# Kernel optimization log

Hardware: AMD Instinct MI355X
Metric: run time of the kernel (lower is better)

Reference implementation:

```python
import jax, jax.numpy as jnp
import numpy as np

N_NODES = 50000
N_EDGES = 800000
NDIM_IN = 64
EDIM = 64
HID = 152  # size_embedding
NDIM_OUT = 64


def _linear(x, W, b):
    # torch nn.Linear: y = x @ W.T + b
    return jnp.matmul(x, W.T) + b


def _sage_layer(nf, ef, Wm, bm, Wa, ba, src, dst):
    # message: gather src node feats, concat edge feats, linear -> [E,1,F]
    m = _linear(jnp.concatenate([nf[src], ef], axis=2), Wm, bm)
    # mean scatter-reduce to dst nodes (zero for nodes with no in-edges)
    s = jax.ops.segment_sum(m, dst, num_segments=N_NODES)
    deg = jax.ops.segment_sum(jnp.ones((m.shape[0],), m.dtype), dst, num_segments=N_NODES)
    h_neigh = s / jnp.maximum(deg, 1.0)[:, None, None]
    # update: concat self + neighbor agg, linear, relu
    return jax.nn.relu(_linear(jnp.concatenate([nf, h_neigh], axis=2), Wa, ba))


def setup_inputs() -> dict:
    key = jax.random.key(0)
    ks = jax.random.split(key, 16)
    def lin_params(kw, kb, fan_in, fan_out):
        bound = 1.0 / np.sqrt(fan_in)
        W = jax.random.uniform(kw, (fan_out, fan_in), jnp.float32, -bound, bound)
        b = jax.random.uniform(kb, (fan_out,), jnp.float32, -bound, bound)
        return W, b
    nfeats = jax.random.normal(ks[0], (N_NODES, 1, NDIM_IN), jnp.float32)
    efeats = jax.random.normal(ks[1], (N_EDGES, 1, EDIM), jnp.float32)
    src = jax.random.randint(ks[2], (N_EDGES,), 0, N_NODES, jnp.int32)
    dst = jax.random.randint(ks[3], (N_EDGES,), 0, N_NODES, jnp.int32)
    Wm1, bm1 = lin_params(ks[4], ks[5], NDIM_IN + EDIM, HID)
    Wa1, ba1 = lin_params(ks[6], ks[7], NDIM_IN + HID, HID)
    Wm2, bm2 = lin_params(ks[8], ks[9], HID + EDIM, HID)
    Wa2, ba2 = lin_params(ks[10], ks[11], HID + HID, HID)
    Wm3, bm3 = lin_params(ks[12], ks[13], HID + EDIM, NDIM_OUT)
    Wa3, ba3 = lin_params(ks[14], ks[15], HID + NDIM_OUT, NDIM_OUT)
    return {
        "nfeats": nfeats, "efeats": efeats,
        "Wm1": Wm1, "bm1": bm1, "Wa1": Wa1, "ba1": ba1,
        "Wm2": Wm2, "bm2": bm2, "Wa2": Wa2, "ba2": ba2,
        "Wm3": Wm3, "bm3": bm3, "Wa3": Wa3, "ba3": ba3,
        "src": src, "dst": dst,
    }


def reference(nfeats, efeats, Wm1, bm1, Wa1, ba1, Wm2, bm2, Wa2, ba2,
              Wm3, bm3, Wa3, ba3, src, dst):
    # dropout is identity in eval mode
    h = _sage_layer(nfeats, efeats, Wm1, bm1, Wa1, ba1, src, dst)
    h = _sage_layer(h, efeats, Wm2, bm2, Wa2, ba2, src, dst)
    h = _sage_layer(h, efeats, Wm3, bm3, Wa3, ba3, src, dst)
    return h.sum(axis=1)  # [N, ndim_out]
```

## Files before the change

### kernel.cpp

```cpp
#include <hip/hip_runtime.h>


#define NN 50000
#define NE 800000
#define NIN 64
#define EDIM_ 64
#define HID_ 152
#define NOUT 64
#define PADN 50176

typedef float f4v __attribute__((ext_vector_type(4)));
typedef _Float16 h8v __attribute__((ext_vector_type(8)));
typedef _Float16 h4v __attribute__((ext_vector_type(4)));

__global__ __launch_bounds__(256) void hist_kernel(const int* __restrict__ dst,
                                                   int* __restrict__ ideg) {
    int e = blockIdx.x * 256 + threadIdx.x;
    if (e < NE) atomicAdd(&ideg[dst[e]], 1);
}

__global__ __launch_bounds__(256) void scan1_kernel(const int* __restrict__ in,
                                                    int* __restrict__ out,
                                                    int* __restrict__ bsum) {
    __shared__ int ws[4];
    int t = threadIdx.x;
    int base = blockIdx.x * 1024 + t * 4;
    int a0 = in[base], a1 = in[base + 1], a2 = in[base + 2], a3 = in[base + 3];
    int s = a0 + a1 + a2 + a3;
    int lane = t & 63, wid = t >> 6;
    int v = s;
#pragma unroll
    for (int d = 1; d < 64; d <<= 1) {
        int u = __shfl_up(v, d);
        if (lane >= d) v += u;
    }
    if (lane == 63) ws[wid] = v;
    __syncthreads();
    int wofs = 0;
    if (wid > 0) wofs += ws[0];
    if (wid > 1) wofs += ws[1];
    if (wid > 2) wofs += ws[2];
    int excl = wofs + v - s;
    out[base] = excl;
    out[base + 1] = excl + a0;
    out[base + 2] = excl + a0 + a1;
    out[base + 3] = excl + a0 + a1 + a2;
    if (t == 255) bsum[blockIdx.x] = wofs + v;
}

__global__ __launch_bounds__(64) void scan2_kernel(int* __restrict__ bsum, int nb) {
    int t = threadIdx.x;
    int orig = (t < nb) ? bsum[t] : 0;
    int v = orig;
#pragma unroll
    for (int d = 1; d < 64; d <<= 1) {
        int u = __shfl_up(v, d);
        if (t >= d) v += u;
    }
    if (t < nb) bsum[t] = v - orig;
}

__global__ __launch_bounds__(256) void scan3_kernel(int* __restrict__ out,
                                                    const int* __restrict__ bsum) {
    int base = blockIdx.x * 1024 + threadIdx.x * 4;
    int b = bsum[blockIdx.x];
    out[base] += b; out[base + 1] += b; out[base + 2] += b; out[base + 3] += b;
}

__global__ __launch_bounds__(256) void scatter_edges_kernel(const int* __restrict__ src,
                                                            const int* __restrict__ dst,
                                                            int* __restrict__ cursor,
                                                            int* __restrict__ csr_nf,
                                                            int* __restrict__ csr_ef) {
    int e = blockIdx.x * 256 + threadIdx.x;
    if (e >= NE) return;
    int d = dst[e];
    int pos = atomicAdd(&cursor[d], 1);
    csr_nf[pos] = src[e];
    csr_ef[pos] = e;
}

template <int F>
__global__ __launch_bounds__(256) void agg_kernel(const float* __restrict__ table,
                                                  const int* __restrict__ rows,
                                                  const int* __restrict__ off,
                                                  float* __restrict__ out) {
    constexpr int C = F / 4;
    constexpr int NPW = 64 / C;
    int t = threadIdx.x;
    int lane = t & 63, wid = t >> 6;
    int sub = lane / C;
    int ch = lane - sub * C;
    int n = (blockIdx.x * 4 + wid) * NPW + sub;
    if (sub >= NPW || n >= NN) return;
    int s = off[n], e = off[n + 1];
    float ax0 = 0.f, ax1 = 0.f, ax2 = 0.f, ax3 = 0.f;
    float bx0 = 0.f, bx1 = 0.f, bx2 = 0.f, bx3 = 0.f;
    int i = s;
    for (; i + 1 < e; i += 2) {
        int r0 = rows[i], r1 = rows[i + 1];
        float4 v0 = *(const float4*)(table + (size_t)r0 * F + ch * 4);
        float4 v1 = *(const float4*)(table + (size_t)r1 * F + ch * 4);
        ax0 += v0.x; ax1 += v0.y; ax2 += v0.z; ax3 += v0.w;
        bx0 += v1.x; bx1 += v1.y; bx2 += v1.z; bx3 += v1.w;
    }
    if (i < e) {
        int r0 = rows[i];
        float4 v0 = *(const float4*)(table + (size_t)r0 * F + ch * 4);
        ax0 += v0.x; ax1 += v0.y; ax2 += v0.z; ax3 += v0.w;
    }
    float4 r;
    r.x = ax0 + bx0; r.y = ax1 + bx1; r.z = ax2 + bx2; r.w = ax3 + bx3;
    *(float4*)(out + (size_t)n * F + ch * 4) = r;
}

__global__ __launch_bounds__(256) void wsplit_kernel(const float* __restrict__ W,
                                                     _Float16* __restrict__ hi,
                                                     _Float16* __restrict__ lo,
                                                     int NT, int Kin1, int K1P,
                                                     int Kin2, int KTP, int total) {
    int e = blockIdx.x * 256 + threadIdx.x;
    if (e >= total) return;
    int n = e / KTP, k = e - n * KTP;
    float v = 0.f;
    if (n < NT) {
        int s = -1;
        if (k < K1P) { if (k < Kin1) s = k; }
        else { int k2 = k - K1P; if (k2 < Kin2) s = Kin1 + k2; }
        if (s >= 0) v = W[(size_t)n * (Kin1 + Kin2) + s];
    }
    _Float16 h = (_Float16)v;
    hi[e] = h;
    lo[e] = (_Float16)(v - (float)h);
}

template <int K1P, int K2P, int K1, int K2, int NT, bool MSG>
__global__ __launch_bounds__(256) void mgemm_kernel(const float* __restrict__ X1,
                                                    const float* __restrict__ X2,
                                                    const _Float16* __restrict__ Whi,
                                                    const _Float16* __restrict__ Wlo,
                                                    const float* __restrict__ bias,
                                                    const int* __restrict__ off,
                                                    float* __restrict__ out) {
    constexpr int KTP = K1P + K2P;
    constexpr int NKS = KTP / 32;
    __shared__ _Float16 sm[12288];

    const int t = threadIdx.x;
    const int m0 = blockIdx.x * 128;
    const int n0 = blockIdx.y * 64;

    const int ar = t >> 3;
    const int akc = (t & 7) * 4;
    const int br = t >> 2;
    const int bkc = (t & 3) * 8;
    const _Float16* wph = Whi + (size_t)(n0 + br) * KTP + bkc;
    const _Float16* wpl = Wlo + (size_t)(n0 + br) * KTP + bkc;

    f4v ax[4];
    h8v bxh, bxl;

    auto loadT = [&](int k0) {
        const float* Xp; int Ka, kb;
        if (k0 < K1P) { Xp = X1; Ka = K1; kb = k0; }
        else          { Xp = X2; Ka = K2; kb = k0 - K1P; }
        const int kg = kb + akc;
        const bool kok = kg < Ka;
        f4v z = {0.f, 0.f, 0.f, 0.f};
#pragma unroll
        for (int i = 0; i < 4; ++i) {
            const int row = m0 + ar + 32 * i;
            ax[i] = (kok && row < NN) ? *(const f4v*)(Xp + (size_t)row * Ka + kg) : z;
        }
        bxh = *(const h8v*)(wph + k0);
        bxl = *(const h8v*)(wpl + k0);
    };
    auto storeT = [&]() {
#pragma unroll
        for (int i = 0; i < 4; ++i) {
            h4v hi, lo;
#pragma unroll
            for (int j = 0; j < 4; ++j) {
                float v = ax[i][j];
                _Float16 h = (_Float16)v;
                hi[j] = h;
                lo[j] = (_Float16)(v - (float)h);
            }
            const int d = (ar + 32 * i) * 32 + akc;
            *(h4v*)(sm + d) = hi;
            *(h4v*)(sm + 4096 + d) = lo;
        }
        const int bd = br * 32 + bkc;
        *(h8v*)(sm + 8192 + bd) = bxh;
        *(h8v*)(sm + 10240 + bd) = bxl;
    };

    const int lane = t & 63, wid = t >> 6;
    const int wm = wid >> 1, wn = wid & 1;
    const int lr = lane & 15, g = lane >> 4;
    const int aoff = (wm * 64 + lr) * 32 + g * 8;
    const int boff = (wn * 32 + lr) * 32 + g * 8;

    f4v acc[4][2] = {};

    loadT(0);
    storeT();
    __syncthreads();

    for (int s = 0; s < NKS; ++s) {
        const bool more = (s + 1 < NKS);
        if (more) loadT((s + 1) * 32);
        h8v ah[4], al[4], bh[2], bl[2];
#pragma unroll
        for (int mf = 0; mf < 4; ++mf) {
            ah[mf] = *(const h8v*)(sm + aoff + mf * 512);
            al[mf] = *(const h8v*)(sm + 4096 + aoff + mf * 512);
        }
#pragma unroll
        for (int nf = 0; nf < 2; ++nf) {
            bh[nf] = *(const h8v*)(sm + 8192 + boff + nf * 512);
            bl[nf] = *(const h8v*)(sm + 10240 + boff + nf * 512);
        }
#pragma unroll
        for (int mf = 0; mf < 4; ++mf)
#pragma unroll
            for (int nf = 0; nf < 2; ++nf) {
                acc[mf][nf] = __builtin_amdgcn_mfma_f32_16x16x32_f16(ah[mf], bh[nf], acc[mf][nf], 0, 0, 0);
                acc[mf][nf] = __builtin_amdgcn_mfma_f32_16x16x32_f16(ah[mf], bl[nf], acc[mf][nf], 0, 0, 0);
                acc[mf][nf] = __builtin_amdgcn_mfma_f32_16x16x32_f16(al[mf], bh[nf], acc[mf][nf], 0, 0, 0);
            }
        if (more) {
            __syncthreads();
            storeT();
            __syncthreads();
        }
    }

#pragma unroll
    for (int mf = 0; mf < 4; ++mf) {
#pragma unroll
        for (int r = 0; r < 4; ++r) {
            const int m = m0 + wm * 64 + mf * 16 + g * 4 + r;
            if (m >= NN) continue;
            float dv = 0.f, inv = 0.f;
            if (MSG) {
                dv = (float)(off[m + 1] - off[m]);
                inv = 1.0f / fmaxf(dv, 1.0f);
            }
#pragma unroll
            for (int nf = 0; nf < 2; ++nf) {
                const int n = n0 + wn * 32 + nf * 16 + lr;
                if (n >= NT) continue;
                const float a = acc[mf][nf][r];
                const float val = MSG ? (a + dv * bias[n]) * inv
                                      : fmaxf(a + bias[n], 0.0f);
                out[(size_t)m * NT + n] = val;
            }
        }
    }
}

extern "C" void kernel_launch(void* const* d_in, const int* in_sizes, int n_in,
                              void* d_out, int out_size, void* d_ws, size_t ws_size,
                              hipStream_t stream) {
    const float* nfeats = (const float*)d_in[0];
    const float* efeats = (const float*)d_in[1];
    const float* Wm1 = (const float*)d_in[2];
    const float* bm1 = (const float*)d_in[3];
    const float* Wa1 = (const float*)d_in[4];
    const float* ba1 = (const float*)d_in[5];
    const float* Wm2 = (const float*)d_in[6];
    const float* bm2 = (const float*)d_in[7];
    const float* Wa2 = (const float*)d_in[8];
    const float* ba2 = (const float*)d_in[9];
    const float* Wm3 = (const float*)d_in[10];
    const float* bm3 = (const float*)d_in[11];
    const float* Wa3 = (const float*)d_in[12];
    const float* ba3 = (const float*)d_in[13];
    const int* src = (const int*)d_in[14];
    const int* dst = (const int*)d_in[15];
    float* out = (float*)d_out;

    int* iws = (int*)d_ws;
    int* ideg   = iws;
    int* off    = iws + PADN;
    int* cursor = iws + 2 * PADN;
    int* csr_nf = iws + 3 * PADN;
    int* csr_ef = csr_nf + NE;
    float* B = (float*)(csr_ef + NE);
    float* P = B + 3200000;
    float* Q = P + 7600000;
    float* R = Q + 7600000;
    _Float16* w1h = (_Float16*)(R + 7600000);
    _Float16* w1l = w1h + 24576;
    _Float16* w2h = w1l + 24576;
    _Float16* w2l = w2h + 43008;
    _Float16* w3h = w2l + 43008;
    _Float16* w3l = w3h + 43008;
    _Float16* w4h = w3l + 43008;
    _Float16* w4l = w4h + 61440;
    _Float16* w5h = w4l + 61440;
    _Float16* w5l = w5h + 14336;
    _Float16* w6h = w5l + 14336;
    _Float16* w6l = w6h + 14336;

    const int BLK = 256;
    auto cdiv = [](long long a, long long b) { return (int)((a + b - 1) / b); };
    dim3 g152(cdiv(NN, 128), 3);
    dim3 g64(cdiv(NN, 128), 1);
    const int NB = PADN / 1024;

    wsplit_kernel<<<96,  BLK, 0, stream>>>(Wm1, w1h, w1l, 152, 64, 64, 64, 128, 24576);
    wsplit_kernel<<<168, BLK, 0, stream>>>(Wa1, w2h, w2l, 152, 64, 64, 152, 224, 43008);
    wsplit_kernel<<<168, BLK, 0, stream>>>(Wm2, w3h, w3l, 152, 152, 160, 64, 224, 43008);
    wsplit_kernel<<<240, BLK, 0, stream>>>(Wa2, w4h, w4l, 152, 152, 160, 152, 320, 61440);
    wsplit_kernel<<<56,  BLK, 0, stream>>>(Wm3, w5h, w5l, 64, 152, 160, 64, 224, 14336);
    wsplit_kernel<<<56,  BLK, 0, stream>>>(Wa3, w6h, w6l, 64, 152, 160, 64, 224, 14336);

    hipMemsetAsync(ideg, 0, (size_t)PADN * 4, stream);
    hist_kernel<<<cdiv(NE, BLK), BLK, 0, stream>>>(dst, ideg);
    scan1_kernel<<<NB, 256, 0, stream>>>(ideg, off, cursor);
    scan2_kernel<<<1, 64, 0, stream>>>(cursor, NB);
    scan3_kernel<<<NB, 256, 0, stream>>>(off, cursor);
    hipMemcpyAsync(cursor, off, (size_t)NN * 4, hipMemcpyDeviceToDevice, stream);
    scatter_edges_kernel<<<cdiv(NE, BLK), BLK, 0, stream>>>(src, dst, cursor, csr_nf, csr_ef);

    agg_kernel<EDIM_><<<cdiv(NN, 16), BLK, 0, stream>>>(efeats, csr_ef, off, B);

    agg_kernel<NIN><<<cdiv(NN, 16), BLK, 0, stream>>>(nfeats, csr_nf, off, P);
    mgemm_kernel<64, 64, 64, 64, HID_, true><<<g152, BLK, 0, stream>>>(P, B, w1h, w1l, bm1, off, Q);
    mgemm_kernel<64, 160, 64, 152, HID_, false><<<g152, BLK, 0, stream>>>(nfeats, Q, w2h, w2l, ba1, off, R);

    agg_kernel<HID_><<<cdiv(NN, 4), BLK, 0, stream>>>(R, csr_nf, off, P);
    mgemm_kernel<160, 64, 152, 64, HID_, true><<<g152, BLK, 0, stream>>>(P, B, w3h, w3l, bm2, off, Q);
    mgemm_kernel<160, 160, 152, 152, HID_, false><<<g152, BLK, 0, stream>>>(R, Q, w4h, w4l, ba2, off, P);

    agg_kernel<HID_><<<cdiv(NN, 4), BLK, 0, stream>>>(P, csr_nf, off, Q);
    mgemm_kernel<160, 64, 152, 64, NOUT, true><<<g64, BLK, 0, stream>>>(Q, B, w5h, w5l, bm3, off, R);
    mgemm_kernel<160, 64, 152, 64, NOUT, false><<<g64, BLK, 0, stream>>>(P, R, w6h, w6l, ba3, off, out);
}
```

Before: 824.6 us.

## Double-buffer LDS tiles with XOR swizzle in split-fp16 GEMM kernel

The dense GEMM kernel now uses two LDS buffers, so the next K-slice is stored while the current one is consumed, which removes one of the two barriers per iteration. LDS writes and reads use an XOR-swizzled layout meant to avoid bank conflicts on the 32-half row stride. Row pointers and offsets are precomputed, the K loop is fully unrolled, and launch bounds request 3 blocks per SM. The cost is doubled LDS use (48KB per block), which may limit occupancy, plus added register pressure.

```diff
diff --git a/kernel.cpp b/kernel.cpp
--- a/kernel.cpp
+++ b/kernel.cpp
@@ -135,47 +135,84 @@
 }
 
 template <int K1P, int K2P, int K1, int K2, int NT, bool MSG>
-__global__ __launch_bounds__(256) void mgemm_kernel(const float* __restrict__ X1,
-                                                    const float* __restrict__ X2,
-                                                    const _Float16* __restrict__ Whi,
-                                                    const _Float16* __restrict__ Wlo,
-                                                    const float* __restrict__ bias,
-                                                    const int* __restrict__ off,
-                                                    float* __restrict__ out) {
+__global__ __launch_bounds__(256, 3) void mgemm_kernel(const float* __restrict__ X1,
+                                                       const float* __restrict__ X2,
+                                                       const _Float16* __restrict__ Whi,
+                                                       const _Float16* __restrict__ Wlo,
+                                                       const float* __restrict__ bias,
+                                                       const int* __restrict__ off,
+                                                       float* __restrict__ out) {
     constexpr int KTP = K1P + K2P;
     constexpr int NKS = KTP / 32;
-    __shared__ _Float16 sm[12288];
+    __shared__ _Float16 sm[2][12288];
 
     const int t = threadIdx.x;
     const int m0 = blockIdx.x * 128;
     const int n0 = blockIdx.y * 64;
 
     const int ar = t >> 3;
-    const int akc = (t & 7) * 4;
+    const int hc = t & 7;
+    const int akc = hc * 4;
     const int br = t >> 2;
-    const int bkc = (t & 3) * 8;
-    const _Float16* wph = Whi + (size_t)(n0 + br) * KTP + bkc;
-    const _Float16* wpl = Wlo + (size_t)(n0 + br) * KTP + bkc;
+    const int cb = t & 3;
+
+    int awofs[4];
+#pragma unroll
+    for (int i = 0; i < 4; ++i) {
+        const int row = ar + 32 * i;
+        awofs[i] = row * 32 + (((hc >> 1) ^ ((row >> 1) & 3)) * 8) + (hc & 1) * 4;
+    }
+    const int bwofs = br * 32 + ((cb ^ ((br >> 1) & 3)) * 8);
+
+    const _Float16* wph = Whi + (size_t)(n0 + br) * KTP + cb * 8;
+    const _Float16* wpl = Wlo + (size_t)(n0 + br) * KTP + cb * 8;
+
+    const float* arp1[4];
+    const float* arp2[4];
+    bool rok[4];
+#pragma unroll
+    for (int i = 0; i < 4; ++i) {
+        const int row = m0 + ar + 32 * i;
+        rok[i] = row < NN;
+        arp1[i] = X1 + (size_t)row * K1;
+        arp2[i] = X2 + (size_t)row * K2;
+    }
+
+    const int lane = t & 63, wid = t >> 6;
+    const int wm = wid >> 1, wn = wid & 1;
+    const int lr = lane & 15, g = lane >> 4;
+    int arofs[4], brofs[2];
+#pragma unroll
+    for (int mf = 0; mf < 4; ++mf) {
+        const int row = wm * 64 + mf * 16 + lr;
+        arofs[mf] = row * 32 + ((g ^ ((row >> 1) & 3)) * 8);
+    }
+#pragma unroll
+    for (int nf = 0; nf < 2; ++nf) {
+        const int row = wn * 32 + nf * 16 + lr;
+        brofs[nf] = row * 32 + ((g ^ ((row >> 1) & 3)) * 8);
+    }
 
     f4v ax[4];
     h8v bxh, bxl;
-
-    auto loadT = [&](int k0) {
-        const float* Xp; int Ka, kb;
-        if (k0 < K1P) { Xp = X1; Ka = K1; kb = k0; }
-        else          { Xp = X2; Ka = K2; kb = k0 - K1P; }
+    f4v acc[4][2] = {};
+
+    auto loadA = [&](const float* const arp[4], const int Ka, const int kb) {
         const int kg = kb + akc;
         const bool kok = kg < Ka;
-        f4v z = {0.f, 0.f, 0.f, 0.f};
-#pragma unroll
-        for (int i = 0; i < 4; ++i) {
-            const int row = m0 + ar + 32 * i;
-            ax[i] = (kok && row < NN) ? *(const f4v*)(Xp + (size_t)row * Ka + kg) : z;
-        }
+        const f4v z = {0.f, 0.f, 0.f, 0.f};
+#pragma unroll
+        for (int i = 0; i < 4; ++i)
+            ax[i] = (kok && rok[i]) ? *(const f4v*)(arp[i] + kg) : z;
+    };
+    auto loadT = [&](int k0) {
+        if (k0 < K1P) loadA(arp1, K1, k0);
+        else          loadA(arp2, K2, k0 - K1P);
         bxh = *(const h8v*)(wph + k0);
         bxl = *(const h8v*)(wpl + k0);
     };
-    auto storeT = [&]() {
+    auto storeT = [&](int buf) {
+        _Float16* s0 = &sm[buf][0];
 #pragma unroll
         for (int i = 0; i < 4; ++i) {
             h4v hi, lo;
@@ -186,40 +223,31 @@
                 hi[j] = h;
                 lo[j] = (_Float16)(v - (float)h);
             }
-            const int d = (ar + 32 * i) * 32 + akc;
-            *(h4v*)(sm + d) = hi;
-            *(h4v*)(sm + 4096 + d) = lo;
-        }
-        const int bd = br * 32 + bkc;
-        *(h8v*)(sm + 8192 + bd) = bxh;
-        *(h8v*)(sm + 10240 + bd) = bxl;
+            *(h4v*)(s0 + awofs[i]) = hi;
+            *(h4v*)(s0 + 4096 + awofs[i]) = lo;
+        }
+        *(h8v*)(s0 + 8192 + bwofs) = bxh;
+        *(h8v*)(s0 + 10240 + bwofs) = bxl;
     };
 
-    const int lane = t & 63, wid = t >> 6;
-    const int wm = wid >> 1, wn = wid & 1;
-    const int lr = lane & 15, g = lane >> 4;
-    const int aoff = (wm * 64 + lr) * 32 + g * 8;
-    const int boff = (wn * 32 + lr) * 32 + g * 8;
-
-    f4v acc[4][2] = {};
-
     loadT(0);
-    storeT();
+    storeT(0);
     __syncthreads();
 
+#pragma unroll
     for (int s = 0; s < NKS; ++s) {
-        const bool more = (s + 1 < NKS);
-        if (more) loadT((s + 1) * 32);
+        if (s + 1 < NKS) loadT((s + 1) * 32);
+        const _Float16* s0 = &sm[s & 1][0];
         h8v ah[4], al[4], bh[2], bl[2];
 #pragma unroll
         for (int mf = 0; mf < 4; ++mf) {
-            ah[mf] = *(const h8v*)(sm + aoff + mf * 512);
-            al[mf] = *(const h8v*)(sm + 4096 + aoff + mf * 512);
+            ah[mf] = *(const h8v*)(s0 + arofs[mf]);
+            al[mf] = *(const h8v*)(s0 + 4096 + arofs[mf]);
         }
 #pragma unroll
         for (int nf = 0; nf < 2; ++nf) {
-            bh[nf] = *(const h8v*)(sm + 8192 + boff + nf * 512);
-            bl[nf] = *(const h8v*)(sm + 10240 + boff + nf * 512);
+            bh[nf] = *(const h8v*)(s0 + 8192 + brofs[nf]);
+            bl[nf] = *(const h8v*)(s0 + 10240 + brofs[nf]);
         }
 #pragma unroll
         for (int mf = 0; mf < 4; ++mf)
@@ -229,9 +257,8 @@
                 acc[mf][nf] = __builtin_amdgcn_mfma_f32_16x16x32_f16(ah[mf], bl[nf], acc[mf][nf], 0, 0, 0);
                 acc[mf][nf] = __builtin_amdgcn_mfma_f32_16x16x32_f16(al[mf], bh[nf], acc[mf][nf], 0, 0, 0);
             }
-        if (more) {
-            __syncthreads();
-            storeT();
+        if (s + 1 < NKS) {
+            storeT((s + 1) & 1);
             __syncthreads();
         }
     }
```

Result: no change. 825.4 us (+0.1%).
